# Performance work log

Hardware: AMD Instinct MI355X
Metric: run time of the kernel (lower is better)

Reference implementation:

```python
import jax, jax.numpy as jnp
import numpy as np

N = 100_000        # num nodes
E = 1_600_000      # num edges (avg degree 16)
F_IN = 128         # input node feature dim
F_E = 32           # edge feature dim
D = 32             # out_dim per head
H = 4              # heads


def setup_inputs() -> dict:
    key = jax.random.key(0)
    ks = jax.random.split(key, 8)
    s = 0.05
    return {
        "node_features": jax.random.normal(ks[0], (N, F_IN), jnp.float32),
        "edge_index": jax.random.randint(ks[1], (E, 2), 0, N, jnp.int32),
        "edge_features": jax.random.normal(ks[2], (E, F_E), jnp.float32),
        "W_node": jax.random.normal(ks[3], (F_IN, D * H), jnp.float32) * s,
        "W_edge": jax.random.normal(ks[4], (F_E, D * H), jnp.float32) * s,
        "attn_kernel": jax.random.normal(ks[5], (H, 3 * D), jnp.float32) * s,
        "W_out": jax.random.normal(ks[6], (D * H, D), jnp.float32) * s,
        "b_out": jnp.zeros((D,), jnp.float32),
    }


def segment_softmax(logits, seg, num_segments):
    # logits: [E, H], seg: [E] destination node ids
    mx = jax.ops.segment_max(logits, seg, num_segments=num_segments)   # [N, H]
    ex = jnp.exp(logits - mx[seg])
    denom = jax.ops.segment_sum(ex, seg, num_segments=num_segments)    # [N, H]
    return ex / (denom[seg] + 1e-8)


def reference(node_features, edge_index, edge_features, W_node, W_edge,
              attn_kernel, W_out, b_out):
    src_idx = edge_index[:, 0]
    dst_idx = edge_index[:, 1]

    # Node / edge projections -> [*, H, D]
    node_proj = (node_features @ W_node).reshape(N, H, D)
    edge_proj = (edge_features @ W_edge).reshape(E, H, D)

    # attn_kernel is [H, 3D] applied to concat(src, dst, edge); split it so we
    # never materialize the [E, H, 3D] concat. Src/dst terms are computed
    # per-node then gathered (same math, far less traffic).
    a_src, a_dst, a_edge = attn_kernel[:, :D], attn_kernel[:, D:2 * D], attn_kernel[:, 2 * D:]
    s_src = jnp.einsum('nhd,hd->nh', node_proj, a_src)   # [N, H]
    s_dst = jnp.einsum('nhd,hd->nh', node_proj, a_dst)   # [N, H]
    s_edge = jnp.einsum('ehd,hd->eh', edge_proj, a_edge)  # [E, H]

    logits = s_src[src_idx] + s_dst[dst_idx] + s_edge     # [E, H]
    attn = segment_softmax(logits, dst_idx, N)             # [E, H]

    src_feat = node_proj[src_idx]                          # [E, H, D]
    messages = (attn[:, :, None] * src_feat).reshape(E, H * D)
    agg = jax.ops.segment_sum(messages, dst_idx, num_segments=N)  # [N, H*D]

    out = jax.nn.gelu(agg @ W_out + b_out, approximate=False)     # exact erf GELU
    return out
```

## Files before the change

### kernel.cpp

```cpp
#include <hip/hip_runtime.h>
#include <hip/hip_bf16.h>
#include <hip/hip_fp16.h>

#define F_IN 128
#define F_E  32
#define DH   128
#define HD   32

__device__ __forceinline__ unsigned short f2bf(float f) {
    unsigned int x = __float_as_uint(f);
    unsigned int r = (x + 0x7fffu + ((x >> 16) & 1u)) >> 16;
    return (unsigned short)r;
}

__global__ void prep_kernel(const float* __restrict__ W_edge,
                            const float* __restrict__ attn,
                            float* __restrict__ wefold) {
    int t = threadIdx.x;
    int f = t >> 2, h = t & 3;
    float s = 0.f;
#pragma unroll
    for (int d = 0; d < 32; ++d)
        s += W_edge[f * DH + h * HD + d] * attn[h * 96 + 64 + d];
    wefold[f * 4 + h] = s;
}

__global__ __launch_bounds__(256, 4)
void node_proj_kernel(const float* __restrict__ x, const float* __restrict__ Wn,
                      const float* __restrict__ attn,
                      unsigned short* __restrict__ proj_bf,
                      float* __restrict__ s_src, int N) {
    __shared__ float xsT[32 * 132];
    __shared__ float ws[32 * 132];
    const int t  = threadIdx.x;
    const int n0 = blockIdx.x * 128;
    const int tc = t & 15, tn = t >> 4;
    const float4* x4  = (const float4*)x;
    const float4* Wn4 = (const float4*)Wn;

    float acc[2][2][4][4];
#pragma unroll
    for (int a = 0; a < 2; ++a)
#pragma unroll
        for (int b = 0; b < 2; ++b)
#pragma unroll
            for (int i = 0; i < 4; ++i)
#pragma unroll
                for (int j = 0; j < 4; ++j) acc[a][b][i][j] = 0.f;

    for (int ch = 0; ch < 4; ++ch) {
        __syncthreads();
#pragma unroll
        for (int j = 0; j < 4; ++j) {
            int idx = t + j * 256;
            int n  = idx >> 3;
            int kq = idx & 7;
            float4 v = make_float4(0.f, 0.f, 0.f, 0.f);
            if (n0 + n < N) v = x4[(size_t)(n0 + n) * 32 + ch * 8 + kq];
            int kk = kq * 4;
            xsT[(kk + 0) * 132 + n] = v.x;
            xsT[(kk + 1) * 132 + n] = v.y;
            xsT[(kk + 2) * 132 + n] = v.z;
            xsT[(kk + 3) * 132 + n] = v.w;
        }
#pragma unroll
        for (int j = 0; j < 4; ++j) {
            int idx = t + j * 256;
            int kk = idx >> 5, cq = idx & 31;
            float4 v = Wn4[(size_t)(ch * 32 + kk) * 32 + cq];
            *(float4*)&ws[kk * 132 + cq * 4] = v;
        }
        __syncthreads();
#pragma unroll 4
        for (int kk = 0; kk < 32; ++kk) {
            float4 a0 = *(const float4*)&xsT[kk * 132 + tn * 4];
            float4 a1 = *(const float4*)&xsT[kk * 132 + 64 + tn * 4];
            float4 b0 = *(const float4*)&ws[kk * 132 + tc * 4];
            float4 b1 = *(const float4*)&ws[kk * 132 + 64 + tc * 4];
            float av[2][4] = {{a0.x, a0.y, a0.z, a0.w}, {a1.x, a1.y, a1.z, a1.w}};
            float bv[2][4] = {{b0.x, b0.y, b0.z, b0.w}, {b1.x, b1.y, b1.z, b1.w}};
#pragma unroll
            for (int ni = 0; ni < 2; ++ni)
#pragma unroll
                for (int ci = 0; ci < 2; ++ci)
#pragma unroll
                    for (int ii = 0; ii < 4; ++ii)
#pragma unroll
                        for (int jj = 0; jj < 4; ++jj)
                            acc[ni][ci][ii][jj] =
                                fmaf(av[ni][ii], bv[ci][jj], acc[ni][ci][ii][jj]);
        }
    }

    float asv[2][4];
#pragma unroll
    for (int ci = 0; ci < 2; ++ci)
#pragma unroll
        for (int jj = 0; jj < 4; ++jj) {
            int c = ci * 64 + tc * 4 + jj;
            int h = c >> 5, d = c & 31;
            asv[ci][jj] = attn[h * 96 + d];
        }

#pragma unroll
    for (int ni = 0; ni < 2; ++ni)
#pragma unroll
        for (int ii = 0; ii < 4; ++ii) {
            int n = n0 + ni * 64 + tn * 4 + ii;
            bool ok = (n < N);
            if (ok) {
                union { unsigned short h[4]; uint2 u; } p0, p1;
#pragma unroll
                for (int jj = 0; jj < 4; ++jj) {
                    p0.h[jj] = f2bf(acc[ni][0][ii][jj]);
                    p1.h[jj] = f2bf(acc[ni][1][ii][jj]);
                }
                *(uint2*)&proj_bf[(size_t)n * DH + tc * 4]      = p0.u;
                *(uint2*)&proj_bf[(size_t)n * DH + 64 + tc * 4] = p1.u;
            }
#pragma unroll
            for (int ci = 0; ci < 2; ++ci) {
                float ps = 0.f;
#pragma unroll
                for (int jj = 0; jj < 4; ++jj)
                    ps = fmaf(acc[ni][ci][ii][jj], asv[ci][jj], ps);
                ps += __shfl_xor(ps, 1);
                ps += __shfl_xor(ps, 2);
                ps += __shfl_xor(ps, 4);
                if (ok && (tc & 7) == 0) {
                    int h = ci * 2 + (tc >> 3);
                    s_src[n * 4 + h] = ps;
                }
            }
        }
}

__global__ __launch_bounds__(256)
void edgeprep_kernel(const float* __restrict__ ef, const int* __restrict__ eidx,
                     const float* __restrict__ wefold,
                     const float* __restrict__ s_src,
                     int* __restrict__ cnt, uint4* __restrict__ rec_e, int E) {
    __shared__ float wf[128];
    const int t = threadIdx.x;
    if (t < 128) wf[t] = wefold[t];
    __syncthreads();

    const int e = blockIdx.x * 256 + t;
    if (e >= E) return;
    int2 sd = ((const int2*)eidx)[e];
    int s_i = sd.x, d_i = sd.y;
    float es0 = 0.f, es1 = 0.f, es2 = 0.f, es3 = 0.f;
#pragma unroll
    for (int f4 = 0; f4 < 8; ++f4) {
        float4 v = *(const float4*)&ef[(size_t)e * F_E + f4 * 4];
        float vv[4] = {v.x, v.y, v.z, v.w};
#pragma unroll
        for (int q = 0; q < 4; ++q) {
            float4 wv = *(const float4*)&wf[(f4 * 4 + q) * 4];
            es0 = fmaf(vv[q], wv.x, es0);
            es1 = fmaf(vv[q], wv.y, es1);
            es2 = fmaf(vv[q], wv.z, es2);
            es3 = fmaf(vv[q], wv.w, es3);
        }
    }
    float4 a = *(const float4*)&s_src[s_i * 4];
    float w0 = __expf(a.x + es0), w1 = __expf(a.y + es1);
    float w2 = __expf(a.z + es2), w3 = __expf(a.w + es3);
    unsigned int u0 = __half_as_ushort(__float2half_rn(w0));
    unsigned int u1 = __half_as_ushort(__float2half_rn(w1));
    unsigned int u2 = __half_as_ushort(__float2half_rn(w2));
    unsigned int u3 = __half_as_ushort(__float2half_rn(w3));
    int r = atomicAdd(&cnt[d_i], 1);
    uint4 R;
    R.x = (unsigned int)s_i;
    R.y = u0 | (u1 << 16);
    R.z = u2 | (u3 << 16);
    R.w = ((unsigned int)d_i << 15) | (unsigned int)r;
    rec_e[e] = R;
}

__global__ __launch_bounds__(256)
void scan1_kernel(const int* __restrict__ cnt, int* __restrict__ cursor,
                  int* __restrict__ bsum, int N) {
    __shared__ int s[256];
    const int t = threadIdx.x;
    int i = blockIdx.x * 256 + t;
    int v = (i < N) ? cnt[i] : 0;
    s[t] = v;
    __syncthreads();
#pragma unroll
    for (int d = 1; d < 256; d <<= 1) {
        int x = (t >= d) ? s[t - d] : 0;
        __syncthreads();
        s[t] += x;
        __syncthreads();
    }
    if (i < N) cursor[i] = s[t] - v;
    if (t == 255) bsum[blockIdx.x] = s[255];
}

__global__ __launch_bounds__(512)
void scan2_kernel(int* __restrict__ bsum, int nb) {
    __shared__ int s[512];
    const int t = threadIdx.x;
    int v = (t < nb) ? bsum[t] : 0;
    s[t] = v;
    __syncthreads();
#pragma unroll
    for (int d = 1; d < 512; d <<= 1) {
        int x = (t >= d) ? s[t - d] : 0;
        __syncthreads();
        s[t] += x;
        __syncthreads();
    }
    if (t < nb) bsum[t] = s[t] - v;
}

__global__ __launch_bounds__(256)
void scatter_kernel(const uint4* __restrict__ rec_e,
                    const int* __restrict__ cursor,
                    const int* __restrict__ bsum,
                    uint4* __restrict__ rec, int E) {
    const int e = blockIdx.x * 256 + threadIdx.x;
    if (e >= E) return;
    uint4 R = rec_e[e];
    int d = (int)(R.w >> 15);
    int r = (int)(R.w & 32767u);
    int pos = cursor[d] + bsum[d >> 8] + r;
    rec[pos] = R;
}

__global__ __launch_bounds__(256)
void gather_kernel(const int* __restrict__ cursor, const int* __restrict__ bsum,
                   const uint4* __restrict__ rec,
                   const unsigned int* __restrict__ proj_bf,
                   unsigned int* __restrict__ numer_bf, int N, int E) {
    const int t    = threadIdx.x;
    const int lane = t & 63;
    const int n    = blockIdx.x * 4 + (t >> 6);
    if (n >= N) return;

    int start = cursor[n] + bsum[n >> 8];
    int end   = (n == N - 1) ? E : (cursor[n + 1] + bsum[(n + 1) >> 8]);
    start = __builtin_amdgcn_readfirstlane(start);
    end   = __builtin_amdgcn_readfirstlane(end);
    const int h = lane >> 4;

    float2 acc = make_float2(0.f, 0.f);
    float dsum = 0.f;

    int i   = start;
    int rem = end - start;
    int c0  = rem < 4 ? rem : 4;
    uint4 ra[4];
#pragma unroll
    for (int q = 0; q < 4; ++q) ra[q] = rec[i + q];

    while (c0 > 0) {
        const int i1   = i + c0;
        const int rem1 = rem - c0;
        const int c1   = rem1 < 4 ? rem1 : 4;
        uint4 rb[4];
#pragma unroll
        for (int q = 0; q < 4; ++q) rb[q] = rec[i1 + q];
        unsigned int pv[4];
#pragma unroll
        for (int q = 0; q < 4; ++q) {
            unsigned int s = (q < c0) ? ra[q].x : 0u;
            pv[q] = proj_bf[(size_t)s * 64 + lane];
        }
#pragma unroll
        for (int q = 0; q < 4; ++q) {
            unsigned int packed = (h < 2) ? ra[q].y : ra[q].z;
            packed = (q < c0) ? packed : 0u;
            unsigned short uw = (h & 1) ? (unsigned short)(packed >> 16)
                                        : (unsigned short)(packed & 0xffffu);
            float w = __half2float(__ushort_as_half(uw));
            dsum += w;
            acc.x = fmaf(w, __uint_as_float(pv[q] << 16), acc.x);
            acc.y = fmaf(w, __uint_as_float(pv[q] & 0xffff0000u), acc.y);
        }
#pragma unroll
        for (int q = 0; q < 4; ++q) ra[q] = rb[q];
        i = i1; rem = rem1; c0 = c1;
    }

    float r = 1.f / (dsum + 1e-8f);
    unsigned int p = (unsigned int)f2bf(acc.x * r) |
                     ((unsigned int)f2bf(acc.y * r) << 16);
    numer_bf[(size_t)n * 64 + lane] = p;
}

__global__ __launch_bounds__(256, 2)
void out_kernel(const unsigned int* __restrict__ numer_bf,
                const float* __restrict__ Wout, const float* __restrict__ bout,
                float* __restrict__ out, int N) {
    __shared__ float wsh[128 * 32];
    __shared__ float bsh[32];
    const int t = threadIdx.x;
    for (int i = t; i < 4096; i += 256) wsh[i] = Wout[i];
    if (t < 32) bsh[t] = bout[t];
    __syncthreads();

    int n = blockIdx.x * 256 + t;
    if (n >= N) return;

    float acc[32];
#pragma unroll
    for (int j = 0; j < 32; ++j) acc[j] = 0.f;

    for (int kg = 0; kg < 16; ++kg) {
        uint4 v = *(const uint4*)&numer_bf[(size_t)n * 64 + kg * 4];
        unsigned int vv[4] = {v.x, v.y, v.z, v.w};
#pragma unroll
        for (int q = 0; q < 4; ++q) {
            int k = kg * 8 + q * 2;
            float a0 = __uint_as_float(vv[q] << 16);
            float a1 = __uint_as_float(vv[q] & 0xffff0000u);
#pragma unroll
            for (int j = 0; j < 32; j += 4) {
                float4 w0 = *(const float4*)&wsh[k * 32 + j];
                float4 w1 = *(const float4*)&wsh[(k + 1) * 32 + j];
                acc[j + 0] = fmaf(a0, w0.x, fmaf(a1, w1.x, acc[j + 0]));
                acc[j + 1] = fmaf(a0, w0.y, fmaf(a1, w1.y, acc[j + 1]));
                acc[j + 2] = fmaf(a0, w0.z, fmaf(a1, w1.z, acc[j + 2]));
                acc[j + 3] = fmaf(a0, w0.w, fmaf(a1, w1.w, acc[j + 3]));
            }
        }
    }
#pragma unroll
    for (int j = 0; j < 32; ++j) {
        float z = acc[j] + bsh[j];
        acc[j] = 0.5f * z * (1.f + erff(z * 0.70710678118654752f));
    }
#pragma unroll
    for (int j = 0; j < 32; j += 4)
        *(float4*)&out[(size_t)n * 32 + j] = make_float4(acc[j], acc[j+1], acc[j+2], acc[j+3]);
}

extern "C" void kernel_launch(void* const* d_in, const int* in_sizes, int n_in,
                              void* d_out, int out_size, void* d_ws, size_t ws_size,
                              hipStream_t stream) {
    const float* x    = (const float*)d_in[0];
    const int*   eidx = (const int*)d_in[1];
    const float* ef   = (const float*)d_in[2];
    const float* Wn   = (const float*)d_in[3];
    const float* We   = (const float*)d_in[4];
    const float* attn = (const float*)d_in[5];
    const float* Wout = (const float*)d_in[6];
    const float* bout = (const float*)d_in[7];
    float* out = (float*)d_out;

    const int N = in_sizes[0] / F_IN;
    const int E = in_sizes[1] / 2;
    const int NB = (N + 255) / 256;

    char* ws = (char*)d_ws;
    size_t off = 0;
    auto alloc = [&](size_t bytes) {
        void* p = ws + off;
        off = (off + bytes + 255) & ~(size_t)255;
        return p;
    };
    int*   cnt     = (int*)  alloc((size_t)N * 4);
    size_t zero_bytes = off;
    int*   cursor  = (int*)  alloc((size_t)N * 4);
    int*   bsum    = (int*)  alloc(512 * 4);
    float* wefold  = (float*)alloc(512);
    float* s_src   = (float*)alloc((size_t)N * 4 * 4);
    unsigned short* proj_bf = (unsigned short*)alloc((size_t)N * DH * 2);
    size_t numer_bytes = (size_t)N * 64 * 4;
    size_t rece_bytes  = (size_t)E * 16;
    unsigned int* numer_bf = (unsigned int*)alloc(numer_bytes > rece_bytes ?
                                                  numer_bytes : rece_bytes);
    uint4* rec_e   = (uint4*)numer_bf;
    uint4* rec     = (uint4*)alloc((size_t)E * 16 + 64);

    hipMemsetAsync(d_ws, 0, zero_bytes, stream);
    hipLaunchKernelGGL(prep_kernel, dim3(1), dim3(128), 0, stream, We, attn, wefold);
    hipLaunchKernelGGL(node_proj_kernel, dim3((N + 127) / 128), dim3(256), 0, stream,
                       x, Wn, attn, proj_bf, s_src, N);
    hipLaunchKernelGGL(edgeprep_kernel, dim3((E + 255) / 256), dim3(256), 0, stream,
                       ef, eidx, wefold, s_src, cnt, rec_e, E);
    hipLaunchKernelGGL(scan1_kernel, dim3(NB), dim3(256), 0, stream, cnt, cursor, bsum, N);
    hipLaunchKernelGGL(scan2_kernel, dim3(1), dim3(512), 0, stream, bsum, NB);
    hipLaunchKernelGGL(scatter_kernel, dim3((E + 255) / 256), dim3(256), 0, stream,
                       rec_e, cursor, bsum, rec, E);
    hipLaunchKernelGGL(gather_kernel, dim3((N + 3) / 4), dim3(256), 0, stream,
                       cursor, bsum, rec, (const unsigned int*)proj_bf, numer_bf, N, E);
    hipLaunchKernelGGL(out_kernel, dim3((N + 255) / 256), dim3(256), 0, stream,
                       numer_bf, Wout, bout, out, N);
}
```

Before: 528.4 us.

## Split wavefront into two half-waves processing alternate edges with 8-byte gathers

The gather kernel now splits each 64-lane wave into two 32-lane halves. Each half handles alternate edges and each lane loads 4 bf16 features (uint2) instead of 2. The edge record prefetch batch grows from 4 to 8, and the two halves' partial sums are combined with a cross-half shuffle before normalisation and store. The aim is more memory-level parallelism per wave on the random source-row gathers, at the cost of extra registers, shuffles and half the lanes idling during the store. The record buffer padding is enlarged to cover the wider prefetch overrun.

```diff
diff --git a/kernel.cpp b/kernel.cpp
--- a/kernel.cpp
+++ b/kernel.cpp
@@ -244,51 +244,70 @@
     int end   = (n == N - 1) ? E : (cursor[n + 1] + bsum[(n + 1) >> 8]);
     start = __builtin_amdgcn_readfirstlane(start);
     end   = __builtin_amdgcn_readfirstlane(end);
-    const int h = lane >> 4;
-
-    float2 acc = make_float2(0.f, 0.f);
+
+    const int hf  = lane >> 5;
+    const int col = lane & 31;
+    const int h   = col >> 3;
+
+    float4 acc = make_float4(0.f, 0.f, 0.f, 0.f);
     float dsum = 0.f;
 
     int i   = start;
     int rem = end - start;
-    int c0  = rem < 4 ? rem : 4;
-    uint4 ra[4];
-#pragma unroll
-    for (int q = 0; q < 4; ++q) ra[q] = rec[i + q];
+    int c0  = rem < 8 ? rem : 8;
+    uint4 ra[8];
+#pragma unroll
+    for (int q = 0; q < 8; ++q) ra[q] = rec[i + q];
 
     while (c0 > 0) {
         const int i1   = i + c0;
         const int rem1 = rem - c0;
-        const int c1   = rem1 < 4 ? rem1 : 4;
-        uint4 rb[4];
-#pragma unroll
-        for (int q = 0; q < 4; ++q) rb[q] = rec[i1 + q];
-        unsigned int pv[4];
-#pragma unroll
-        for (int q = 0; q < 4; ++q) {
-            unsigned int s = (q < c0) ? ra[q].x : 0u;
-            pv[q] = proj_bf[(size_t)s * 64 + lane];
-        }
-#pragma unroll
-        for (int q = 0; q < 4; ++q) {
-            unsigned int packed = (h < 2) ? ra[q].y : ra[q].z;
-            packed = (q < c0) ? packed : 0u;
-            unsigned short uw = (h & 1) ? (unsigned short)(packed >> 16)
-                                        : (unsigned short)(packed & 0xffffu);
+        const int c1   = rem1 < 8 ? rem1 : 8;
+        uint4 rb[8];
+#pragma unroll
+        for (int q = 0; q < 8; ++q) rb[q] = rec[i1 + q];
+        uint2 pv[4];
+        unsigned int wp[4];
+#pragma unroll
+        for (int j = 0; j < 4; ++j) {
+            bool v = (2 * j + hf) < c0;
+            unsigned int sx = hf ? ra[2 * j + 1].x : ra[2 * j].x;
+            unsigned int py = hf ? ra[2 * j + 1].y : ra[2 * j].y;
+            unsigned int pz = hf ? ra[2 * j + 1].z : ra[2 * j].z;
+            sx = v ? sx : 0u;
+            unsigned int pk = (h < 2) ? py : pz;
+            wp[j] = v ? pk : 0u;
+            pv[j] = *(const uint2*)&proj_bf[(size_t)sx * 64 + col * 2];
+        }
+#pragma unroll
+        for (int j = 0; j < 4; ++j) {
+            unsigned short uw = (h & 1) ? (unsigned short)(wp[j] >> 16)
+                                        : (unsigned short)(wp[j] & 0xffffu);
             float w = __half2float(__ushort_as_half(uw));
             dsum += w;
-            acc.x = fmaf(w, __uint_as_float(pv[q] << 16), acc.x);
-            acc.y = fmaf(w, __uint_as_float(pv[q] & 0xffff0000u), acc.y);
-        }
-#pragma unroll
-        for (int q = 0; q < 4; ++q) ra[q] = rb[q];
+            acc.x = fmaf(w, __uint_as_float(pv[j].x << 16), acc.x);
+            acc.y = fmaf(w, __uint_as_float(pv[j].x & 0xffff0000u), acc.y);
+            acc.z = fmaf(w, __uint_as_float(pv[j].y << 16), acc.z);
+            acc.w = fmaf(w, __uint_as_float(pv[j].y & 0xffff0000u), acc.w);
+        }
+#pragma unroll
+        for (int q = 0; q < 8; ++q) ra[q] = rb[q];
         i = i1; rem = rem1; c0 = c1;
     }
 
-    float r = 1.f / (dsum + 1e-8f);
-    unsigned int p = (unsigned int)f2bf(acc.x * r) |
-                     ((unsigned int)f2bf(acc.y * r) << 16);
-    numer_bf[(size_t)n * 64 + lane] = p;
+    dsum  += __shfl_xor(dsum, 32);
+    acc.x += __shfl_xor(acc.x, 32);
+    acc.y += __shfl_xor(acc.y, 32);
+    acc.z += __shfl_xor(acc.z, 32);
+    acc.w += __shfl_xor(acc.w, 32);
+
+    if (hf == 0) {
+        float r = 1.f / (dsum + 1e-8f);
+        uint2 p;
+        p.x = (unsigned int)f2bf(acc.x * r) | ((unsigned int)f2bf(acc.y * r) << 16);
+        p.y = (unsigned int)f2bf(acc.z * r) | ((unsigned int)f2bf(acc.w * r) << 16);
+        *(uint2*)&numer_bf[(size_t)n * 64 + col * 2] = p;
+    }
 }
 
 __global__ __launch_bounds__(256, 2)
@@ -374,7 +393,7 @@
     unsigned int* numer_bf = (unsigned int*)alloc(numer_bytes > rece_bytes ?
                                                   numer_bytes : rece_bytes);
     uint4* rec_e   = (uint4*)numer_bf;
-    uint4* rec     = (uint4*)alloc((size_t)E * 16 + 64);
+    uint4* rec     = (uint4*)alloc((size_t)E * 16 + 128);
 
     hipMemsetAsync(d_ws, 0, zero_bytes, stream);
     hipLaunchKernelGGL(prep_kernel, dim3(1), dim3(128), 0, stream, We, attn, wefold);
```

Result: slower. 1.077 ms (+103.9%).
